# Kernel tuning notes

Measured on AMD Instinct MI355X. Metric: run time of the kernel, lower is better.

## Reference

```python
import jax, jax.numpy as jnp
import numpy as np

EPS = 1e-5
K = 20
NEG_SLOPE = 0.2


def lrelu(x):
    return jnp.where(x >= 0, x, NEG_SLOPE * x)


def bn_train(x, w, b, axes):
    # training-mode batch norm (biased variance), channel axis = 1
    m = jnp.mean(x, axis=axes, keepdims=True)
    v = jnp.mean((x - m) ** 2, axis=axes, keepdims=True)
    shp = [1] * x.ndim
    shp[1] = -1
    return (x - m) * jax.lax.rsqrt(v + EPS) * w.reshape(shp) + b.reshape(shp)


def knn_idx(x, k):
    # x: [B, C, N] -> idx [B, N, k] of k nearest neighbors (max of -dist^2)
    inner = -2.0 * jnp.einsum('bcn,bcm->bnm', x, x)
    xx = jnp.sum(x * x, axis=1)  # [B, N]
    pd = -xx[:, None, :] - inner - xx[:, :, None]  # [B, N, N]
    return jax.lax.top_k(pd, k)[1]


def graph_feature(x, k):
    # x: [B, C, N] -> [B, 2C, N, k] = cat(neighbor - center, center)
    B = x.shape[0]
    idx = knn_idx(x, k)  # [B, N, k]
    xt = jnp.transpose(x, (0, 2, 1))  # [B, N, C]
    nbr = xt[jnp.arange(B)[:, None, None], idx]  # [B, N, k, C] gather
    ctr = jnp.broadcast_to(xt[:, :, None, :], nbr.shape)
    feat = jnp.concatenate([nbr - ctr, ctr], axis=-1)  # [B, N, k, 2C]
    return jnp.transpose(feat, (0, 3, 1, 2))


def edge_conv(x, w, bw, bb):
    # EdgeConv: graph feature -> 1x1 conv (no bias) -> BN -> LeakyReLU -> max over k
    f = graph_feature(x, K)                      # [B, 2C, N, k]
    y = jnp.einsum('bcnk,oc->bonk', f, w)        # 1x1 conv2d
    y = lrelu(bn_train(y, bw, bb, (0, 2, 3)))
    return jnp.max(y, axis=-1)                   # [B, O, N]


def setup_inputs() -> dict:
    key = jax.random.key(0)
    ks = jax.random.split(key, 12)
    B, N = 8, 1024
    s = 0.05
    inp = {'x': jax.random.normal(ks[0], (B, 3, N), dtype=jnp.float32)}
    inp['c1w'] = jax.random.normal(ks[1], (64, 6), dtype=jnp.float32) * s
    inp['c2w'] = jax.random.normal(ks[2], (64, 128), dtype=jnp.float32) * s
    inp['c3w'] = jax.random.normal(ks[3], (128, 128), dtype=jnp.float32) * s
    inp['c4w'] = jax.random.normal(ks[4], (256, 256), dtype=jnp.float32) * s
    inp['c5w'] = jax.random.normal(ks[5], (1024, 512), dtype=jnp.float32) * s
    for i, c in zip(range(1, 8), [64, 64, 128, 256, 1024, 512, 256]):
        inp[f'b{i}w'] = jnp.ones((c,), dtype=jnp.float32)
        inp[f'b{i}b'] = jnp.zeros((c,), dtype=jnp.float32)
    inp['l1w'] = jax.random.normal(ks[6], (512, 2048), dtype=jnp.float32) * s
    inp['l1b'] = jnp.zeros((512,), dtype=jnp.float32)
    inp['l2w'] = jax.random.normal(ks[7], (256, 512), dtype=jnp.float32) * s
    inp['l2b'] = jnp.zeros((256,), dtype=jnp.float32)
    inp['l3w'] = jax.random.normal(ks[8], (40, 256), dtype=jnp.float32) * s
    inp['l3b'] = jnp.zeros((40,), dtype=jnp.float32)
    return inp


def reference(x, c1w, c2w, c3w, c4w, c5w,
              b1w, b1b, b2w, b2b, b3w, b3b, b4w, b4b, b5w, b5b,
              b6w, b6b, b7w, b7b,
              l1w, l1b, l2w, l2b, l3w, l3b):
    x1 = edge_conv(x, c1w, b1w, b1b)    # [B, 64, N]
    x2 = edge_conv(x1, c2w, b2w, b2b)   # [B, 64, N]
    x3 = edge_conv(x2, c3w, b3w, b3b)   # [B, 128, N]
    x4 = edge_conv(x3, c4w, b4w, b4b)   # [B, 256, N]
    cat = jnp.concatenate([x1, x2, x3, x4], axis=1)  # [B, 512, N]
    y = jnp.einsum('bcn,oc->bon', cat, c5w)          # conv5 (1x1)
    y = lrelu(bn_train(y, b5w, b5b, (0, 2)))         # [B, 1024, N]
    feat = jnp.concatenate([jnp.max(y, axis=-1), jnp.mean(y, axis=-1)], axis=1)  # [B, 2048]
    h = feat @ l1w.T + l1b
    h = lrelu(bn_train(h, b6w, b6b, (0,)))
    h = h @ l2w.T + l2b
    h = lrelu(bn_train(h, b7w, b7b, (0,)))
    return h @ l3w.T + l3b  # [B, num_class]
```

## Files before the change

### kernel.cpp

```cpp
#include <hip/hip_runtime.h>
#include <math.h>

#define NPTS 1024
#define NBATCH 8
#define KNN 20
#define KC 24
#define EPSBN 1e-5f
#define NSLOPE 0.2f

typedef __attribute__((ext_vector_type(8))) short short8_t;
typedef __attribute__((ext_vector_type(4))) float floatx4;

__device__ __forceinline__ float lrelu_f(float x){ return x >= 0.f ? x : NSLOPE*x; }

__device__ __forceinline__ unsigned short f2bf_rne(float f){
  union { float f; unsigned u; } x; x.f = f;
  unsigned r = x.u + 0x7FFFu + ((x.u >> 16) & 1u);
  return (unsigned short)(r >> 16);
}
__device__ __forceinline__ float bf2f(unsigned short h){
  union { float f; unsigned u; } x; x.u = ((unsigned)h) << 16;
  return x.f;
}

__global__ __launch_bounds__(256) void pd_gemm64(const float* __restrict__ X, long bstride,
                                                 int coff, int C, float* __restrict__ PD){
  __shared__ float As[16][68];
  __shared__ float Bs[16][68];
  int b = blockIdx.z;
  int r0 = blockIdx.y * 64;
  int q0 = blockIdx.x * 64;
  int t = threadIdx.x;
  const float* Xb = X + (size_t)b*bstride + (size_t)coff*NPTS;
  float acc[4][4] = {};
  float xm2[4] = {};
  int lr = t >> 4, lc = (t & 15) << 2;
  int tr = (t >> 4) << 2, tc = (t & 15) << 2;
  for (int k0 = 0; k0 < C; k0 += 16){
    float4 av = make_float4(0,0,0,0), bv = make_float4(0,0,0,0);
    if (k0 + lr < C){
      const float* rp = Xb + (size_t)(k0+lr)*NPTS;
      av = *(const float4*)(rp + r0 + lc);
      bv = *(const float4*)(rp + q0 + lc);
    }
    *(float4*)&As[lr][lc] = av;
    *(float4*)&Bs[lr][lc] = bv;
    __syncthreads();
    #pragma unroll
    for (int kk = 0; kk < 16; ++kk){
      float4 a4 = *(const float4*)&As[kk][tr];
      float4 b4 = *(const float4*)&Bs[kk][tc];
      float a[4] = {a4.x,a4.y,a4.z,a4.w};
      float bb[4] = {b4.x,b4.y,b4.z,b4.w};
      #pragma unroll
      for (int j = 0; j < 4; ++j) xm2[j] += bb[j]*bb[j];
      #pragma unroll
      for (int i = 0; i < 4; ++i)
        #pragma unroll
        for (int j = 0; j < 4; ++j) acc[i][j] += a[i]*bb[j];
    }
    __syncthreads();
  }
  #pragma unroll
  for (int i = 0; i < 4; ++i){
    size_t base = ((size_t)b*NPTS + r0 + tr + i)*NPTS + q0 + tc;
    *(float4*)(PD + base) = make_float4(2.f*acc[i][0]-xm2[0], 2.f*acc[i][1]-xm2[1],
                                        2.f*acc[i][2]-xm2[2], 2.f*acc[i][3]-xm2[3]);
  }
}

__global__ void xt_kernel(const float* __restrict__ X, long bstride, int coff, int C,
                          float* __restrict__ XT){
  __shared__ float tile[32][33];
  int b = blockIdx.z;
  int c0 = blockIdx.y * 32;
  int n0 = blockIdx.x * 32;
  int t = threadIdx.x;
  int r = t >> 3, q = t & 7;
  float4 rv = *(const float4*)(X + (size_t)b*bstride + (size_t)(coff+c0+r)*NPTS + n0 + q*4);
  tile[r][q*4+0] = rv.x; tile[r][q*4+1] = rv.y; tile[r][q*4+2] = rv.z; tile[r][q*4+3] = rv.w;
  __syncthreads();
  float4 ov = make_float4(tile[q*4+0][r], tile[q*4+1][r], tile[q*4+2][r], tile[q*4+3][r]);
  *(float4*)(XT + ((size_t)b*NPTS + n0 + r)*C + c0 + q*4) = ov;
}

__global__ __launch_bounds__(256) void topk_refine(const float* __restrict__ PD,
                                                   const float* __restrict__ X, long bstride,
                                                   int coff, int C,
                                                   const float* __restrict__ XT,
                                                   int* __restrict__ IDX){
  int wid = threadIdx.x >> 6;
  int lane = threadIdx.x & 63;
  int row = blockIdx.x*4 + wid;
  int b = row >> 10, n = row & 1023;
  const float* p = PD + (size_t)row*NPTS;
  unsigned key[16];
  #pragma unroll
  for (int j4 = 0; j4 < 4; ++j4){
    float4 t4 = *(const float4*)&p[lane*16 + j4*4];
    float tv[4] = {t4.x, t4.y, t4.z, t4.w};
    #pragma unroll
    for (int e = 0; e < 4; ++e){
      int j = j4*4 + e;
      unsigned u = __float_as_uint(tv[e]);
      unsigned msk = (unsigned)(((int)u) >> 31) | 0x80000000u;
      key[j] = ((u ^ msk) & 0xFFFFFFF0u) | (unsigned)j;
    }
  }
  #pragma unroll
  for (int ksz = 2; ksz <= 16; ksz <<= 1){
    #pragma unroll
    for (int jj = ksz >> 1; jj > 0; jj >>= 1){
      #pragma unroll
      for (int i = 0; i < 16; ++i){
        int l = i ^ jj;
        if (l > i){
          unsigned a = key[i], c = key[l];
          unsigned mx = a > c ? a : c, mn = a > c ? c : a;
          bool maxfirst = ((i & ksz) == 0);
          key[i] = maxfirst ? mx : mn;
          key[l] = maxfirst ? mn : mx;
        }
      }
    }
  }
  int my_m = 0;
  #pragma unroll
  for (int k = 0; k < KC; ++k){
    unsigned h = key[0];
    unsigned gm = h;
    #pragma unroll
    for (int m = 1; m < 64; m <<= 1){
      unsigned o = (unsigned)__shfl_xor((int)gm, m, 64);
      gm = (o > gm) ? o : gm;
    }
    unsigned long long ball = __ballot(h == gm);
    int wl = __ffsll((unsigned long long)ball) - 1;
    if (lane == k) my_m = wl*16 + (int)(gm & 15u);
    bool isw = (lane == wl);
    #pragma unroll
    for (int i2 = 0; i2 < 15; ++i2) key[i2] = isw ? key[i2+1] : key[i2];
    key[15] = isw ? 0u : key[15];
  }
  double pdv = -1e300; int midx = 1 << 20;
  if (lane < KC){
    midx = my_m;
    double dot = 0.0, m2 = 0.0, n2 = 0.0;
    if (C == 3){
      const float* Xb = X + (size_t)b*bstride + (size_t)coff*NPTS;
      #pragma unroll
      for (int c = 0; c < 3; ++c){
        double xn = (double)Xb[(size_t)c*NPTS + n];
        double xm = (double)Xb[(size_t)c*NPTS + my_m];
        dot += xn*xm; m2 += xm*xm; n2 += xn*xn;
      }
    } else {
      const float* rn = XT + ((size_t)b*NPTS + n)*C;
      const float* rm = XT + ((size_t)b*NPTS + my_m)*C;
      for (int c = 0; c < C; c += 4){
        float4 xn4 = *(const float4*)&rn[c];
        float4 xm4 = *(const float4*)&rm[c];
        dot += (double)xn4.x*(double)xm4.x + (double)xn4.y*(double)xm4.y
             + (double)xn4.z*(double)xm4.z + (double)xn4.w*(double)xm4.w;
        m2  += (double)xm4.x*(double)xm4.x + (double)xm4.y*(double)xm4.y
             + (double)xm4.z*(double)xm4.z + (double)xm4.w*(double)xm4.w;
        n2  += (double)xn4.x*(double)xn4.x + (double)xn4.y*(double)xn4.y
             + (double)xn4.z*(double)xn4.z + (double)xn4.w*(double)xn4.w;
      }
    }
    pdv = (2.0*dot - m2) - n2;
  }
  int rank = 0;
  #pragma unroll
  for (int j = 0; j < KC; ++j){
    double ov = __shfl(pdv, j, 64);
    int    oi = __shfl(midx, j, 64);
    rank += (ov > pdv || (ov == pdv && oi < midx)) ? 1 : 0;
  }
  if (lane < KC && rank < KNN) IDX[(size_t)row*KNN + rank] = midx;
}

__global__ __launch_bounds__(256) void lin_gemm64(const float* __restrict__ W, int M, int Cdim,
                                                  int lda, int O,
                                                  const float* __restrict__ X, long bstride,
                                                  int coff, float* __restrict__ OUT){
  __shared__ float As[16][68];
  __shared__ float Bs[16][68];
  int b = blockIdx.z;
  int m0 = blockIdx.y * 64;
  int n0 = blockIdx.x * 64;
  int t = threadIdx.x;
  const float* Xb = X + (size_t)b*bstride + (size_t)coff*NPTS;
  float acc[4][4] = {};
  int lr = t >> 4, lc = (t & 15) << 2;
  int tr = (t >> 4) << 2, tc = (t & 15) << 2;
  for (int k0 = 0; k0 < Cdim; k0 += 16){
    int c = k0 + lr;
    float4 av = make_float4(0,0,0,0);
    if (c < Cdim){
      #pragma unroll
      for (int j = 0; j < 4; ++j){
        int m = m0 + lc + j;
        float aval = (m < O) ? W[(size_t)m*lda + c]
                             : W[(size_t)(m-O)*lda + Cdim + c] - W[(size_t)(m-O)*lda + c];
        ((float*)&av)[j] = aval;
      }
    }
    float4 bv = make_float4(0,0,0,0);
    if (c < Cdim)
      bv = *(const float4*)(Xb + (size_t)c*NPTS + n0 + lc);
    *(float4*)&As[lr][lc] = av;
    *(float4*)&Bs[lr][lc] = bv;
    __syncthreads();
    #pragma unroll
    for (int kk = 0; kk < 16; ++kk){
      float4 a4 = *(const float4*)&As[kk][tr];
      float4 b4 = *(const float4*)&Bs[kk][tc];
      float a[4] = {a4.x,a4.y,a4.z,a4.w};
      float bb[4] = {b4.x,b4.y,b4.z,b4.w};
      #pragma unroll
      for (int i = 0; i < 4; ++i)
        #pragma unroll
        for (int j = 0; j < 4; ++j) acc[i][j] += a[i]*bb[j];
    }
    __syncthreads();
  }
  #pragma unroll
  for (int i = 0; i < 4; ++i){
    int m = m0 + tr + i;
    *(float4*)(OUT + ((size_t)b*M + m)*NPTS + n0 + tc) =
        make_float4(acc[i][0],acc[i][1],acc[i][2],acc[i][3]);
  }
}

__global__ void edge_stats(const float* __restrict__ V, const int* __restrict__ IDX, int O,
                           float* __restrict__ YMX, float* __restrict__ YMN,
                           float* __restrict__ S1P, float* __restrict__ S2P){
  __shared__ float vrow[NPTS];
  __shared__ float urow[NPTS];
  __shared__ float r1[256];
  __shared__ float r2[256];
  int b = blockIdx.x / O;
  int o = blockIdx.x % O;
  int t = threadIdx.x;
  const float* vp = V + ((size_t)b*2*O + o)*NPTS;
  const float* up = V + ((size_t)b*2*O + O + o)*NPTS;
  for (int i = 0; i < 4; ++i){ vrow[t+256*i] = vp[t+256*i]; urow[t+256*i] = up[t+256*i]; }
  __syncthreads();
  float s1 = 0.f, s2 = 0.f;
  size_t obase = ((size_t)b*O + o)*NPTS;
  for (int i = 0; i < 4; ++i){
    int n = t + 256*i;
    float un = urow[n];
    const int* ip = IDX + ((size_t)b*NPTS + n)*KNN;
    float mx = -1e38f, mn = 1e38f;
    #pragma unroll
    for (int k = 0; k < KNN; ++k){
      float val = un + vrow[ip[k]];
      mx = fmaxf(mx, val); mn = fminf(mn, val);
      s1 += val; s2 += val*val;
    }
    YMX[obase + n] = mx;
    YMN[obase + n] = mn;
  }
  r1[t] = s1; r2[t] = s2;
  __syncthreads();
  for (int s = 128; s > 0; s >>= 1){
    if (t < s){ r1[t] += r1[t+s]; r2[t] += r2[t+s]; }
    __syncthreads();
  }
  if (t == 0){ S1P[b*O + o] = r1[0]; S2P[b*O + o] = r2[0]; }
}

__global__ void edge_apply(const float* __restrict__ YMX, const float* __restrict__ YMN,
                           const float* __restrict__ S1P, const float* __restrict__ S2P,
                           const float* __restrict__ gw, const float* __restrict__ gb,
                           int O, float* __restrict__ CAT, int coff_out){
  int g = blockIdx.x*blockDim.x + threadIdx.x;
  int n = g & (NPTS-1);
  int o = (g >> 10) % O;
  int b = (g >> 10) / O;
  float s1 = 0.f, s2 = 0.f;
  #pragma unroll
  for (int i = 0; i < NBATCH; ++i){ s1 += S1P[i*O + o]; s2 += S2P[i*O + o]; }
  const float cnt = (float)(NBATCH*NPTS*KNN);
  float mean = s1 / cnt;
  float var = fmaxf(s2 / cnt - mean*mean, 0.f);
  float sc = gw[o] * rsqrtf(var + EPSBN);
  float sh = gb[o] - mean*sc;
  float v = (sc >= 0.f) ? YMX[g] : YMN[g];
  CAT[((size_t)b*512 + coff_out + o)*NPTS + n] = lrelu_f(sc*v + sh);
}

__global__ void wsplit(const float* __restrict__ W, int nelem,
                       unsigned short* __restrict__ Wh, unsigned short* __restrict__ Wl){
  int i = blockIdx.x*blockDim.x + threadIdx.x;
  if (i >= nelem) return;
  float f = W[i];
  unsigned short hi = f2bf_rne(f);
  Wh[i] = hi;
  Wl[i] = f2bf_rne(f - bf2f(hi));
}

__global__ void catsplit_t(const float* __restrict__ CAT,
                           unsigned short* __restrict__ Th, unsigned short* __restrict__ Tl){
  __shared__ float tile[32][33];
  int b = blockIdx.z;
  int c0 = blockIdx.y * 32;
  int n0 = blockIdx.x * 32;
  int t = threadIdx.x;
  int r = t >> 3, q = t & 7;
  float4 rv = *(const float4*)(CAT + ((size_t)b*512 + c0 + r)*NPTS + n0 + q*4);
  tile[r][q*4+0] = rv.x; tile[r][q*4+1] = rv.y; tile[r][q*4+2] = rv.z; tile[r][q*4+3] = rv.w;
  __syncthreads();
  ushort4 oh, ol;
  float f0 = tile[q*4+0][r], f1 = tile[q*4+1][r], f2 = tile[q*4+2][r], f3 = tile[q*4+3][r];
  oh.x = f2bf_rne(f0); ol.x = f2bf_rne(f0 - bf2f(oh.x));
  oh.y = f2bf_rne(f1); ol.y = f2bf_rne(f1 - bf2f(oh.y));
  oh.z = f2bf_rne(f2); ol.z = f2bf_rne(f2 - bf2f(oh.z));
  oh.w = f2bf_rne(f3); ol.w = f2bf_rne(f3 - bf2f(oh.w));
  size_t ob = ((size_t)b*NPTS + n0 + r)*512 + c0 + q*4;
  *(ushort4*)(Th + ob) = oh;
  *(ushort4*)(Tl + ob) = ol;
}

#define LROW 40
__global__ __launch_bounds__(256) void conv5_mfma(
    const unsigned short* __restrict__ Ath, const unsigned short* __restrict__ Atl,
    const unsigned short* __restrict__ Wh,  const unsigned short* __restrict__ Wl,
    float* __restrict__ OUT){
  __shared__ __align__(16) unsigned short Ah[128*LROW];
  __shared__ __align__(16) unsigned short Al[128*LROW];
  __shared__ __align__(16) unsigned short Bh[128*LROW];
  __shared__ __align__(16) unsigned short Bl[128*LROW];
  int b  = blockIdx.z;
  int n0 = blockIdx.x * 128;
  int m0 = blockIdx.y * 128;
  int t = threadIdx.x;
  int lane = t & 63, wid = t >> 6;
  int wn = (wid & 1) * 64;
  int wm = (wid >> 1) * 64;
  int fr = lane & 15;
  int fq = (lane >> 4) * 8;
  floatx4 acc[4][4];
  #pragma unroll
  for (int i = 0; i < 4; ++i)
    #pragma unroll
    for (int j = 0; j < 4; ++j) acc[i][j] = (floatx4)(0.f);

  for (int k0 = 0; k0 < 512; k0 += 32){
    #pragma unroll
    for (int c = 0; c < 2; ++c){
      int ch = t + 256*c;
      int row = ch >> 2, part = (ch & 3)*8;
      size_t ga = ((size_t)b*NPTS + n0 + row)*512 + k0 + part;
      size_t gb = ((size_t)(m0 + row))*512 + k0 + part;
      *(short8_t*)&Ah[row*LROW + part] = *(const short8_t*)&Ath[ga];
      *(short8_t*)&Al[row*LROW + part] = *(const short8_t*)&Atl[ga];
      *(short8_t*)&Bh[row*LROW + part] = *(const short8_t*)&Wh[gb];
      *(short8_t*)&Bl[row*LROW + part] = *(const short8_t*)&Wl[gb];
    }
    __syncthreads();
    short8_t afh[4], afl[4], bfh[4], bfl[4];
    #pragma unroll
    for (int ni = 0; ni < 4; ++ni){
      int r = (wn + ni*16 + fr)*LROW + fq;
      afh[ni] = *(const short8_t*)&Ah[r];
      afl[ni] = *(const short8_t*)&Al[r];
    }
    #pragma unroll
    for (int mi = 0; mi < 4; ++mi){
      int r = (wm + mi*16 + fr)*LROW + fq;
      bfh[mi] = *(const short8_t*)&Bh[r];
      bfl[mi] = *(const short8_t*)&Bl[r];
    }
    #pragma unroll
    for (int ni = 0; ni < 4; ++ni)
      #pragma unroll
      for (int mi = 0; mi < 4; ++mi){
        acc[ni][mi] = __builtin_amdgcn_mfma_f32_16x16x32_bf16(afh[ni], bfh[mi], acc[ni][mi], 0, 0, 0);
        acc[ni][mi] = __builtin_amdgcn_mfma_f32_16x16x32_bf16(afl[ni], bfh[mi], acc[ni][mi], 0, 0, 0);
        acc[ni][mi] = __builtin_amdgcn_mfma_f32_16x16x32_bf16(afh[ni], bfl[mi], acc[ni][mi], 0, 0, 0);
      }
    __syncthreads();
  }
  int col = lane & 15;
  int rquad = (lane >> 4) * 4;
  #pragma unroll
  for (int ni = 0; ni < 4; ++ni)
    #pragma unroll
    for (int mi = 0; mi < 4; ++mi){
      int m = m0 + wm + mi*16 + col;
      int n = n0 + wn + ni*16 + rquad;
      *(floatx4*)(OUT + ((size_t)b*1024 + m)*NPTS + n) = acc[ni][mi];
    }
}

__global__ void y5_stats(const float* __restrict__ Y5, float* __restrict__ S1, float* __restrict__ S2){
  __shared__ float r1[256], r2[256];
  int o = blockIdx.x;
  int t = threadIdx.x;
  float s1 = 0.f, s2 = 0.f;
  for (int b = 0; b < NBATCH; ++b){
    const float* p = Y5 + ((size_t)b*1024 + o)*NPTS;
    for (int n = t; n < NPTS; n += 256){ float v = p[n]; s1 += v; s2 += v*v; }
  }
  r1[t] = s1; r2[t] = s2;
  __syncthreads();
  for (int s = 128; s > 0; s >>= 1){
    if (t < s){ r1[t] += r1[t+s]; r2[t] += r2[t+s]; }
    __syncthreads();
  }
  if (t == 0){ S1[o] = r1[0]; S2[o] = r2[0]; }
}

__global__ void head_kernel(const float* __restrict__ Y5, const float* __restrict__ S1,
                            const float* __restrict__ S2,
                            const float* __restrict__ gw, const float* __restrict__ gb,
                            float* __restrict__ FEAT){
  __shared__ float rm[256], rs[256];
  int o = blockIdx.x & 1023;
  int b = blockIdx.x >> 10;
  int t = threadIdx.x;
  const float cnt = (float)(NBATCH*NPTS);
  float mean = S1[o] / cnt;
  float var = fmaxf(S2[o] / cnt - mean*mean, 0.f);
  float s = gw[o] * rsqrtf(var + EPSBN);
  float sh = gb[o] - mean*s;
  const float* p = Y5 + ((size_t)b*1024 + o)*NPTS;
  float mx = -1e38f, sm = 0.f;
  for (int n = t; n < NPTS; n += 256){
    float v = lrelu_f(s*p[n] + sh);
    mx = fmaxf(mx, v); sm += v;
  }
  rm[t] = mx; rs[t] = sm;
  __syncthreads();
  for (int st = 128; st > 0; st >>= 1){
    if (t < st){ rm[t] = fmaxf(rm[t], rm[t+st]); rs[t] += rs[t+st]; }
    __syncthreads();
  }
  if (t == 0){
    FEAT[(size_t)b*2048 + o]        = rm[0];
    FEAT[(size_t)b*2048 + 1024 + o] = rs[0] * (1.f/NPTS);
  }
}

__global__ void fc_bn(const float* __restrict__ IN, int ID, int OD,
                      const float* __restrict__ W, const float* __restrict__ bias,
                      const float* __restrict__ gw, const float* __restrict__ gb,
                      float* __restrict__ OUT){
  __shared__ float red[256][8];
  int f = blockIdx.x;
  int t = threadIdx.x;
  float acc[8] = {};
  const float* wr = W + (size_t)f*ID;
  for (int j = t; j < ID; j += 256){
    float wv = wr[j];
    #pragma unroll
    for (int b = 0; b < 8; ++b) acc[b] += IN[b*ID + j] * wv;
  }
  #pragma unroll
  for (int b = 0; b < 8; ++b) red[t][b] = acc[b];
  __syncthreads();
  for (int s = 128; s > 0; s >>= 1){
    if (t < s){
      #pragma unroll
      for (int b = 0; b < 8; ++b) red[t][b] += red[t+s][b];
    }
    __syncthreads();
  }
  if (t == 0){
    float h[8], mean = 0.f;
    #pragma unroll
    for (int b = 0; b < 8; ++b){ h[b] = red[0][b] + bias[f]; mean += h[b]; }
    mean *= 0.125f;
    float var = 0.f;
    #pragma unroll
    for (int b = 0; b < 8; ++b){ float d = h[b]-mean; var += d*d; }
    var *= 0.125f;
    float sc = gw[f]*rsqrtf(var + EPSBN);
    float sh = gb[f] - mean*sc;
    #pragma unroll
    for (int b = 0; b < 8; ++b) OUT[b*OD + f] = lrelu_f(sc*h[b] + sh);
  }
}

__global__ void fc_out(const float* __restrict__ IN, const float* __restrict__ W,
                       const float* __restrict__ bias, float* __restrict__ OUT){
  __shared__ float red[256][8];
  int j = blockIdx.x;
  int t = threadIdx.x;
  float wv = W[(size_t)j*256 + t];
  #pragma unroll
  for (int b = 0; b < 8; ++b) red[t][b] = IN[b*256 + t] * wv;
  __syncthreads();
  for (int s = 128; s > 0; s >>= 1){
    if (t < s){
      #pragma unroll
      for (int b = 0; b < 8; ++b) red[t][b] += red[t+s][b];
    }
    __syncthreads();
  }
  if (t == 0){
    #pragma unroll
    for (int b = 0; b < 8; ++b) OUT[b*40 + j] = red[0][b] + bias[j];
  }
}

extern "C" void kernel_launch(void* const* d_in, const int* in_sizes, int n_in,
                              void* d_out, int out_size, void* d_ws, size_t ws_size,
                              hipStream_t stream) {
  const float* x   = (const float*)d_in[0];
  const float* cw[5] = { (const float*)d_in[1], (const float*)d_in[2], (const float*)d_in[3],
                         (const float*)d_in[4], (const float*)d_in[5] };
  const float* bw[7]; const float* bbv[7];
  for (int i = 0; i < 7; ++i){ bw[i] = (const float*)d_in[6+2*i]; bbv[i] = (const float*)d_in[7+2*i]; }
  const float* l1w = (const float*)d_in[20]; const float* l1b = (const float*)d_in[21];
  const float* l2w = (const float*)d_in[22]; const float* l2b = (const float*)d_in[23];
  const float* l3w = (const float*)d_in[24]; const float* l3b = (const float*)d_in[25];
  float* out = (float*)d_out;

  float* ws = (float*)d_ws;
  float* PD    = ws;
  float* V     = ws;
  float* YMX   = ws + 4194304;
  float* YMN   = ws + 6291456;
  float* Y5    = ws;
  float* XT    = ws + 8388608;
  unsigned short* CATth = (unsigned short*)(ws + 8388608);
  unsigned short* CATtl = (unsigned short*)(ws + 10485760);
  unsigned short* WhP   = (unsigned short*)(ws + 12582912);
  unsigned short* WlP   = (unsigned short*)(ws + 12845056);
  float* CAT   = ws + 16777216;
  int*   IDX   = (int*)(ws + 20987904);
  float* S1P   = ws + 21151744;
  float* S2P   = ws + 21159936;
  float* FEAT  = ws + 21170176;
  float* H1    = ws + 21186560;
  float* H2    = ws + 21190656;

  struct L { int C, O; const float* in; long bs; int ci; const float* w; int bn; int co; };
  L ls[4] = {
    { 3,   64, x,   (long)3*NPTS,   0,   cw[0], 0, 0   },
    { 64,  64, CAT, (long)512*NPTS, 0,   cw[1], 1, 64  },
    { 64, 128, CAT, (long)512*NPTS, 64,  cw[2], 2, 128 },
    { 128,256, CAT, (long)512*NPTS, 128, cw[3], 3, 256 },
  };

  for (int li = 0; li < 4; ++li){
    L& l = ls[li];
    pd_gemm64<<<dim3(16,16,NBATCH), 256, 0, stream>>>(l.in, l.bs, l.ci, l.C, PD);
    if (l.C >= 32)
      xt_kernel<<<dim3(32, l.C/32, NBATCH), 256, 0, stream>>>(l.in, l.bs, l.ci, l.C, XT);
    topk_refine<<<(NBATCH*NPTS)/4, 256, 0, stream>>>(PD, l.in, l.bs, l.ci, l.C, XT, IDX);
    lin_gemm64<<<dim3(16, (2*l.O)/64, NBATCH), 256, 0, stream>>>(
        l.w, 2*l.O, l.C, 2*l.C, l.O, l.in, l.bs, l.ci, V);
    edge_stats<<<NBATCH*l.O, 256, 0, stream>>>(V, IDX, l.O, YMX, YMN, S1P, S2P);
    edge_apply<<<(NBATCH*l.O*NPTS)/256, 256, 0, stream>>>(
        YMX, YMN, S1P, S2P, bw[l.bn], bbv[l.bn], l.O, CAT, l.co);
  }

  wsplit<<<(1024*512+255)/256, 256, 0, stream>>>(cw[4], 1024*512, WhP, WlP);
  catsplit_t<<<dim3(32,16,NBATCH), 256, 0, stream>>>(CAT, CATth, CATtl);
  conv5_mfma<<<dim3(8,8,NBATCH), 256, 0, stream>>>(CATth, CATtl, WhP, WlP, Y5);

  y5_stats<<<1024, 256, 0, stream>>>(Y5, S1P, S2P);
  head_kernel<<<NBATCH*1024, 256, 0, stream>>>(Y5, S1P, S2P, bw[4], bbv[4], FEAT);

  fc_bn<<<512, 256, 0, stream>>>(FEAT, 2048, 512, l1w, l1b, bw[5], bbv[5], H1);
  fc_bn<<<256, 256, 0, stream>>>(H1, 512, 256, l2w, l2b, bw[6], bbv[6], H2);
  fc_out<<<40, 256, 0, stream>>>(H2, l3w, l3b, out);
}
```

Before: 533.2 us.

## Compute kNN distances with split-bf16 MFMA and threshold-select top-k candidates

The FP32 SIMT pairwise-distance GEMM is replaced by a bf16 hi/lo split MFMA GEMM. It needs a new transpose-and-split kernel and a separate squared-norm kernel. The top-k candidate step no longer does a per-lane bitonic sort plus 24 rounds of wave argmax. It binary-searches a threshold so that between 24 and 64 candidates survive, compacts them into shared memory, and ranks them with the exact double-precision recompute. This cuts distance-matrix compute and selection cost, but adds extra launches, lower-precision candidate scoring, and a 64-wide rank loop.

```diff
diff --git a/kernel.cpp b/kernel.cpp
--- a/kernel.cpp
+++ b/kernel.cpp
@@ -4,7 +4,6 @@
 #define NPTS 1024
 #define NBATCH 8
 #define KNN 20
-#define KC 24
 #define EPSBN 1e-5f
 #define NSLOPE 0.2f
 
@@ -23,50 +22,114 @@
   return x.f;
 }
 
-__global__ __launch_bounds__(256) void pd_gemm64(const float* __restrict__ X, long bstride,
-                                                 int coff, int C, float* __restrict__ PD){
-  __shared__ float As[16][68];
-  __shared__ float Bs[16][68];
+__global__ void xsplit_t(const float* __restrict__ X, long bstride, int coff, int C, int Cp,
+                         unsigned short* __restrict__ Sh, unsigned short* __restrict__ Sl){
+  __shared__ float tile[32][33];
   int b = blockIdx.z;
-  int r0 = blockIdx.y * 64;
-  int q0 = blockIdx.x * 64;
-  int t = threadIdx.x;
-  const float* Xb = X + (size_t)b*bstride + (size_t)coff*NPTS;
-  float acc[4][4] = {};
-  float xm2[4] = {};
-  int lr = t >> 4, lc = (t & 15) << 2;
-  int tr = (t >> 4) << 2, tc = (t & 15) << 2;
-  for (int k0 = 0; k0 < C; k0 += 16){
-    float4 av = make_float4(0,0,0,0), bv = make_float4(0,0,0,0);
-    if (k0 + lr < C){
-      const float* rp = Xb + (size_t)(k0+lr)*NPTS;
-      av = *(const float4*)(rp + r0 + lc);
-      bv = *(const float4*)(rp + q0 + lc);
-    }
-    *(float4*)&As[lr][lc] = av;
-    *(float4*)&Bs[lr][lc] = bv;
-    __syncthreads();
-    #pragma unroll
-    for (int kk = 0; kk < 16; ++kk){
-      float4 a4 = *(const float4*)&As[kk][tr];
-      float4 b4 = *(const float4*)&Bs[kk][tc];
-      float a[4] = {a4.x,a4.y,a4.z,a4.w};
-      float bb[4] = {b4.x,b4.y,b4.z,b4.w};
+  int c0 = blockIdx.y * 32;
+  int n0 = blockIdx.x * 32;
+  int t = threadIdx.x;
+  int r = t >> 3, q = t & 7;
+  float4 rv = make_float4(0,0,0,0);
+  if (c0 + r < C)
+    rv = *(const float4*)(X + (size_t)b*bstride + (size_t)(coff+c0+r)*NPTS + n0 + q*4);
+  tile[r][q*4+0] = rv.x; tile[r][q*4+1] = rv.y; tile[r][q*4+2] = rv.z; tile[r][q*4+3] = rv.w;
+  __syncthreads();
+  ushort4 oh, ol;
+  float f0 = tile[q*4+0][r], f1 = tile[q*4+1][r], f2 = tile[q*4+2][r], f3 = tile[q*4+3][r];
+  oh.x = f2bf_rne(f0); ol.x = f2bf_rne(f0 - bf2f(oh.x));
+  oh.y = f2bf_rne(f1); ol.y = f2bf_rne(f1 - bf2f(oh.y));
+  oh.z = f2bf_rne(f2); ol.z = f2bf_rne(f2 - bf2f(oh.z));
+  oh.w = f2bf_rne(f3); ol.w = f2bf_rne(f3 - bf2f(oh.w));
+  size_t ob = ((size_t)b*NPTS + n0 + r)*Cp + c0 + q*4;
+  *(ushort4*)(Sh + ob) = oh;
+  *(ushort4*)(Sl + ob) = ol;
+}
+
+__global__ void xx32(const float* __restrict__ X, long bstride, int coff, int C,
+                     float* __restrict__ XX){
+  int g = blockIdx.x*blockDim.x + threadIdx.x;
+  int n = g & (NPTS-1);
+  int b = g >> 10;
+  const float* p = X + (size_t)b*bstride + (size_t)coff*NPTS + n;
+  float s = 0.f;
+  for (int c = 0; c < C; ++c){ float v = p[(size_t)c*NPTS]; s += v*v; }
+  XX[g] = s;
+}
+
+#define LROW 40
+__global__ __launch_bounds__(256) void pd_mfma(
+    const unsigned short* __restrict__ Sh, const unsigned short* __restrict__ Sl,
+    int Cp, const float* __restrict__ XX, float* __restrict__ PD){
+  __shared__ __align__(16) unsigned short Ah[128*LROW];
+  __shared__ __align__(16) unsigned short Al[128*LROW];
+  __shared__ __align__(16) unsigned short Bh[128*LROW];
+  __shared__ __align__(16) unsigned short Bl[128*LROW];
+  int b  = blockIdx.z;
+  int n0 = blockIdx.x * 128;
+  int m0 = blockIdx.y * 128;
+  int t = threadIdx.x;
+  int lane = t & 63, wid = t >> 6;
+  int wm = (wid & 1) * 64;
+  int wn = (wid >> 1) * 64;
+  int fr = lane & 15;
+  int fq = (lane >> 4) * 8;
+  floatx4 acc[4][4];
+  #pragma unroll
+  for (int i = 0; i < 4; ++i)
+    #pragma unroll
+    for (int j = 0; j < 4; ++j) acc[i][j] = (floatx4)(0.f);
+
+  for (int k0 = 0; k0 < Cp; k0 += 32){
+    #pragma unroll
+    for (int c = 0; c < 2; ++c){
+      int ch = t + 256*c;
+      int row = ch >> 2, part = (ch & 3)*8;
+      size_t ga = ((size_t)b*NPTS + m0 + row)*Cp + k0 + part;
+      size_t gb = ((size_t)b*NPTS + n0 + row)*Cp + k0 + part;
+      *(short8_t*)&Ah[row*LROW + part] = *(const short8_t*)&Sh[ga];
+      *(short8_t*)&Al[row*LROW + part] = *(const short8_t*)&Sl[ga];
+      *(short8_t*)&Bh[row*LROW + part] = *(const short8_t*)&Sh[gb];
+      *(short8_t*)&Bl[row*LROW + part] = *(const short8_t*)&Sl[gb];
+    }
+    __syncthreads();
+    short8_t afh[4], afl[4], bfh[4], bfl[4];
+    #pragma unroll
+    for (int mi = 0; mi < 4; ++mi){
+      int r = (wm + mi*16 + fr)*LROW + fq;
+      afh[mi] = *(const short8_t*)&Ah[r];
+      afl[mi] = *(const short8_t*)&Al[r];
+    }
+    #pragma unroll
+    for (int ni = 0; ni < 4; ++ni){
+      int r = (wn + ni*16 + fr)*LROW + fq;
+      bfh[ni] = *(const short8_t*)&Bh[r];
+      bfl[ni] = *(const short8_t*)&Bl[r];
+    }
+    #pragma unroll
+    for (int mi = 0; mi < 4; ++mi)
       #pragma unroll
-      for (int j = 0; j < 4; ++j) xm2[j] += bb[j]*bb[j];
-      #pragma unroll
-      for (int i = 0; i < 4; ++i)
-        #pragma unroll
-        for (int j = 0; j < 4; ++j) acc[i][j] += a[i]*bb[j];
-    }
-    __syncthreads();
-  }
-  #pragma unroll
-  for (int i = 0; i < 4; ++i){
-    size_t base = ((size_t)b*NPTS + r0 + tr + i)*NPTS + q0 + tc;
-    *(float4*)(PD + base) = make_float4(2.f*acc[i][0]-xm2[0], 2.f*acc[i][1]-xm2[1],
-                                        2.f*acc[i][2]-xm2[2], 2.f*acc[i][3]-xm2[3]);
-  }
+      for (int ni = 0; ni < 4; ++ni){
+        acc[mi][ni] = __builtin_amdgcn_mfma_f32_16x16x32_bf16(afh[mi], bfh[ni], acc[mi][ni], 0, 0, 0);
+        acc[mi][ni] = __builtin_amdgcn_mfma_f32_16x16x32_bf16(afl[mi], bfh[ni], acc[mi][ni], 0, 0, 0);
+        acc[mi][ni] = __builtin_amdgcn_mfma_f32_16x16x32_bf16(afh[mi], bfl[ni], acc[mi][ni], 0, 0, 0);
+      }
+    __syncthreads();
+  }
+  int col = lane & 15;
+  int rquad = (lane >> 4) * 4;
+  #pragma unroll
+  for (int mi = 0; mi < 4; ++mi)
+    #pragma unroll
+    for (int ni = 0; ni < 4; ++ni){
+      int n = n0 + wn + ni*16 + col;
+      int mbase = m0 + wm + mi*16 + rquad;
+      float4 xx4 = *(const float4*)(XX + (size_t)b*NPTS + mbase);
+      floatx4 a = acc[mi][ni];
+      float4 o = make_float4(2.f*a.x - xx4.x, 2.f*a.y - xx4.y,
+                             2.f*a.z - xx4.z, 2.f*a.w - xx4.w);
+      *(float4*)(PD + ((size_t)b*NPTS + n)*NPTS + mbase) = o;
+    }
 }
 
 __global__ void xt_kernel(const float* __restrict__ X, long bstride, int coff, int C,
@@ -89,6 +152,7 @@
                                                    int coff, int C,
                                                    const float* __restrict__ XT,
                                                    int* __restrict__ IDX){
+  __shared__ int cands[4][64];
   int wid = threadIdx.x >> 6;
   int lane = threadIdx.x & 63;
   int row = blockIdx.x*4 + wid;
@@ -101,49 +165,46 @@
     float tv[4] = {t4.x, t4.y, t4.z, t4.w};
     #pragma unroll
     for (int e = 0; e < 4; ++e){
-      int j = j4*4 + e;
       unsigned u = __float_as_uint(tv[e]);
       unsigned msk = (unsigned)(((int)u) >> 31) | 0x80000000u;
-      key[j] = ((u ^ msk) & 0xFFFFFFF0u) | (unsigned)j;
-    }
-  }
-  #pragma unroll
-  for (int ksz = 2; ksz <= 16; ksz <<= 1){
-    #pragma unroll
-    for (int jj = ksz >> 1; jj > 0; jj >>= 1){
-      #pragma unroll
-      for (int i = 0; i < 16; ++i){
-        int l = i ^ jj;
-        if (l > i){
-          unsigned a = key[i], c = key[l];
-          unsigned mx = a > c ? a : c, mn = a > c ? c : a;
-          bool maxfirst = ((i & ksz) == 0);
-          key[i] = maxfirst ? mx : mn;
-          key[l] = maxfirst ? mn : mx;
-        }
-      }
-    }
-  }
-  int my_m = 0;
-  #pragma unroll
-  for (int k = 0; k < KC; ++k){
-    unsigned h = key[0];
-    unsigned gm = h;
-    #pragma unroll
-    for (int m = 1; m < 64; m <<= 1){
-      unsigned o = (unsigned)__shfl_xor((int)gm, m, 64);
-      gm = (o > gm) ? o : gm;
-    }
-    unsigned long long ball = __ballot(h == gm);
-    int wl = __ffsll((unsigned long long)ball) - 1;
-    if (lane == k) my_m = wl*16 + (int)(gm & 15u);
-    bool isw = (lane == wl);
-    #pragma unroll
-    for (int i2 = 0; i2 < 15; ++i2) key[i2] = isw ? key[i2+1] : key[i2];
-    key[15] = isw ? 0u : key[15];
-  }
-  double pdv = -1e300; int midx = 1 << 20;
-  if (lane < KC){
+      key[j4*4+e] = u ^ msk;
+    }
+  }
+  unsigned lo = 0u, hi = 0xFFFFFFFFu;
+  for (int it = 0; it < 32; ++it){
+    unsigned mid = lo + ((hi - lo) >> 1);
+    int c = 0;
+    #pragma unroll
+    for (int j = 0; j < 16; ++j) c += (key[j] > mid) ? 1 : 0;
+    #pragma unroll
+    for (int m = 1; m < 64; m <<= 1) c += __shfl_xor(c, m, 64);
+    if (c >= 24){ lo = mid; if (c <= 64) break; }
+    else hi = mid;
+  }
+  unsigned T = lo;
+  int ci = 0;
+  #pragma unroll
+  for (int j = 0; j < 16; ++j) ci += (key[j] > T) ? 1 : 0;
+  int sc = ci;
+  #pragma unroll
+  for (int d = 1; d < 64; d <<= 1){
+    int v = __shfl_up(sc, d, 64);
+    if (lane >= d) sc += v;
+  }
+  int base = sc - ci;
+  int total = __shfl(sc, 63, 64);
+  if (total > 64) total = 64;
+  int slot = base;
+  #pragma unroll
+  for (int j = 0; j < 16; ++j){
+    bool surv = key[j] > T;
+    if (surv && slot < 64) cands[wid][slot] = lane*16 + j;
+    slot += surv ? 1 : 0;
+  }
+  __syncthreads();
+  double pdv = -1e300; int midx = (1 << 20) + lane;
+  if (lane < total){
+    int my_m = cands[wid][lane];
     midx = my_m;
     double dot = 0.0, m2 = 0.0, n2 = 0.0;
     if (C == 3){
@@ -171,13 +232,12 @@
     pdv = (2.0*dot - m2) - n2;
   }
   int rank = 0;
-  #pragma unroll
-  for (int j = 0; j < KC; ++j){
+  for (int j = 0; j < 64; ++j){
     double ov = __shfl(pdv, j, 64);
     int    oi = __shfl(midx, j, 64);
     rank += (ov > pdv || (ov == pdv && oi < midx)) ? 1 : 0;
   }
-  if (lane < KC && rank < KNN) IDX[(size_t)row*KNN + rank] = midx;
+  if (lane < total && rank < KNN) IDX[(size_t)row*KNN + rank] = midx;
 }
 
 __global__ __launch_bounds__(256) void lin_gemm64(const float* __restrict__ W, int M, int Cdim,
@@ -324,7 +384,6 @@
   *(ushort4*)(Tl + ob) = ol;
 }
 
-#define LROW 40
 __global__ __launch_bounds__(256) void conv5_mfma(
     const unsigned short* __restrict__ Ath, const unsigned short* __restrict__ Atl,
     const unsigned short* __restrict__ Wh,  const unsigned short* __restrict__ Wl,
@@ -527,6 +586,9 @@
   float* YMN   = ws + 6291456;
   float* Y5    = ws;
   float* XT    = ws + 8388608;
+  unsigned short* XSH = (unsigned short*)(ws + 9437184);
+  unsigned short* XSL = (unsigned short*)(ws + 9961472);
+  float* XX    = ws + 10485760;
   unsigned short* CATth = (unsigned short*)(ws + 8388608);
   unsigned short* CATtl = (unsigned short*)(ws + 10485760);
   unsigned short* WhP   = (unsigned short*)(ws + 12582912);
@@ -539,17 +601,19 @@
   float* H1    = ws + 21186560;
   float* H2    = ws + 21190656;
 
-  struct L { int C, O; const float* in; long bs; int ci; const float* w; int bn; int co; };
+  struct L { int C, Cp, O; const float* in; long bs; int ci; const float* w; int bn; int co; };
   L ls[4] = {
-    { 3,   64, x,   (long)3*NPTS,   0,   cw[0], 0, 0   },
-    { 64,  64, CAT, (long)512*NPTS, 0,   cw[1], 1, 64  },
-    { 64, 128, CAT, (long)512*NPTS, 64,  cw[2], 2, 128 },
-    { 128,256, CAT, (long)512*NPTS, 128, cw[3], 3, 256 },
+    { 3,   32,  64, x,   (long)3*NPTS,   0,   cw[0], 0, 0   },
+    { 64,  64,  64, CAT, (long)512*NPTS, 0,   cw[1], 1, 64  },
+    { 64,  64, 128, CAT, (long)512*NPTS, 64,  cw[2], 2, 128 },
+    { 128, 128,256, CAT, (long)512*NPTS, 128, cw[3], 3, 256 },
   };
 
   for (int li = 0; li < 4; ++li){
     L& l = ls[li];
-    pd_gemm64<<<dim3(16,16,NBATCH), 256, 0, stream>>>(l.in, l.bs, l.ci, l.C, PD);
+    xsplit_t<<<dim3(32, l.Cp/32, NBATCH), 256, 0, stream>>>(l.in, l.bs, l.ci, l.C, l.Cp, XSH, XSL);
+    xx32<<<(NBATCH*NPTS)/256, 256, 0, stream>>>(l.in, l.bs, l.ci, l.C, XX);
+    pd_mfma<<<dim3(8,8,NBATCH), 256, 0, stream>>>(XSH, XSL, l.Cp, XX, PD);
     if (l.C >= 32)
       xt_kernel<<<dim3(32, l.C/32, NBATCH), 256, 0, stream>>>(l.in, l.bs, l.ci, l.C, XT);
     topk_refine<<<(NBATCH*NPTS)/4, 256, 0, stream>>>(PD, l.in, l.bs, l.ci, l.C, XT, IDX);
```

Measured after the change: 613.2 us. +15.0%, slower.
